# Kernel optimization log

Measured on AMD Instinct MI355X. Metric: run time of the kernel, lower is better.

## Reference

```python
import jax, jax.numpy as jnp
import numpy as np

B, H, LQ, LK, D = 2, 16, 2048, 2048, 128

def setup_inputs() -> dict:
    key = jax.random.key(0)
    k1, k2, k3 = jax.random.split(key, 3)
    q = jax.random.normal(k1, (B, H, LQ, D), dtype=jnp.float32)
    k = jax.random.normal(k2, (B, H, LK, D), dtype=jnp.float32)
    v = jax.random.normal(k3, (B, H, LK, D), dtype=jnp.float32)
    return {"q": q, "k": k, "v": v}

def reference(q, k, v):
    # scaled dot-product attention: softmax(q k^T / sqrt(D)) v
    scale = q.shape[-1] ** (-0.5)
    # scores: [B,H,Lq,Lk]
    scores = jnp.einsum('bhqd,bhkd->bhqk', q, k) * scale
    attn = jax.nn.softmax(scores, axis=-1)
    out = jnp.einsum('bhqk,bhkd->bhqd', attn, v)  # [B,H,Lq,Dv]
    return out
```

## Files before the change

kernel.cpp:

```cpp
#include <hip/hip_runtime.h>
#include <hip/hip_bf16.h>
#include <cstdint>

#define LQ_N   2048
#define LK_N   2048
#define DD     128
#define NHEADS 32
#define QBLK   128
#define KVBLK  64
#define NKV    (LK_N / KVBLK)
#define NQB    (LQ_N / QBLK)
#define SCALE  0.08838834764831845f
#define SCALE2 0.1275525003267101f

#define KTILE_BYTES (KVBLK * DD * 2)
#define WS_K_BYTES  ((size_t)NHEADS * NKV * KTILE_BYTES)
#define WS_NEED     (2 * WS_K_BYTES)

#define PSTR 72

typedef __attribute__((ext_vector_type(8)))  short bf16x8;
typedef __attribute__((ext_vector_type(4)))  float f32x4;
typedef __attribute__((ext_vector_type(16))) float f32x16;

#if __has_builtin(__builtin_amdgcn_exp2f)
#define EXP2F __builtin_amdgcn_exp2f
#else
#define EXP2F exp2f
#endif

__device__ inline unsigned short f2bf(float f) {
    union { float f; unsigned u; } x; x.f = f;
    unsigned r = (x.u + 0x7fffu + ((x.u >> 16) & 1u)) >> 16;
    return (unsigned short)r;
}

__device__ inline unsigned cvt_pk_bf16(float lo, float hi) {
    unsigned r;
    asm("v_cvt_pk_bf16_f32 %0, %1, %2" : "=v"(r) : "v"(lo), "v"(hi));
    return r;
}

__device__ inline bf16x8 make_pfrag(float v0, float v1, float v2, float v3,
                                    float v4, float v5, float v6, float v7) {
    unsigned a0 = cvt_pk_bf16(v0, v1);
    unsigned a1 = cvt_pk_bf16(v2, v3);
    unsigned b0 = cvt_pk_bf16(v4, v5);
    unsigned b1 = cvt_pk_bf16(v6, v7);
    asm volatile("v_permlane32_swap_b32 %0, %1" : "+v"(a0), "+v"(b0));
    asm volatile("v_permlane32_swap_b32 %0, %1" : "+v"(a1), "+v"(b1));
    union { unsigned u[4]; bf16x8 v8; } u;
    u.u[0] = a0; u.u[1] = a1; u.u[2] = b0; u.u[3] = b1;
    return u.v8;
}

__global__ __launch_bounds__(256, 2)
void prep_k_kernel(const float* __restrict__ K, char* __restrict__ ws)
{
    const int tid  = threadIdx.x;
    const int kvt  = blockIdx.x;
    const int head = blockIdx.y;
    const float* Kh = K + ((size_t)head * LK_N + (size_t)kvt * KVBLK) * DD;
    char* dst = ws + ((size_t)head * NKV + kvt) * KTILE_BYTES;
    #pragma unroll
    for (int i = 0; i < 4; ++i) {
        int c = tid + 256 * i;
        int row  = c >> 4;
        int col8 = c & 15;
        const float* src = Kh + (size_t)row * DD + col8 * 8;
        float4 a = *(const float4*)src;
        float4 b = *(const float4*)(src + 4);
        bf16x8 t;
        t[0] = (short)f2bf(a.x * SCALE2); t[1] = (short)f2bf(a.y * SCALE2);
        t[2] = (short)f2bf(a.z * SCALE2); t[3] = (short)f2bf(a.w * SCALE2);
        t[4] = (short)f2bf(b.x * SCALE2); t[5] = (short)f2bf(b.y * SCALE2);
        t[6] = (short)f2bf(b.z * SCALE2); t[7] = (short)f2bf(b.w * SCALE2);
        *(bf16x8*)(dst + row * 256 + ((col8 * 16) ^ ((row & 7) << 4))) = t;
    }
}

__global__ __launch_bounds__(256, 2)
void prep_vt_kernel(const float* __restrict__ V, char* __restrict__ ws)
{
    __shared__ unsigned short vt[DD * PSTR];
    const int tid  = threadIdx.x;
    const int kvt  = blockIdx.x;
    const int head = blockIdx.y;
    const float* Vh = V + ((size_t)head * LK_N + (size_t)kvt * KVBLK) * DD;
    #pragma unroll
    for (int i = 0; i < 8; ++i) {
        int f = tid + 256 * i;
        int r  = f >> 5;
        int c4 = f & 31;
        float4 x = *(const float4*)(Vh + (size_t)r * DD + c4 * 4);
        vt[(c4 * 4 + 0) * PSTR + r] = f2bf(x.x);
        vt[(c4 * 4 + 1) * PSTR + r] = f2bf(x.y);
        vt[(c4 * 4 + 2) * PSTR + r] = f2bf(x.z);
        vt[(c4 * 4 + 3) * PSTR + r] = f2bf(x.w);
    }
    __syncthreads();
    char* dst = ws + WS_K_BYTES + ((size_t)head * NKV + kvt) * KTILE_BYTES;
    #pragma unroll
    for (int i = 0; i < 4; ++i) {
        int c = tid + 256 * i;
        int d   = c >> 3;
        int kv8 = c & 7;
        bf16x8 t = *(const bf16x8*)&vt[d * PSTR + kv8 * 8];
        *(bf16x8*)(dst + d * 128 + ((kv8 * 16) ^ ((d & 7) << 4))) = t;
    }
}

__global__ __launch_bounds__(256, 2)
void attn_main_kernel(const float* __restrict__ Q, const char* __restrict__ kws,
                      const char* __restrict__ vws, float* __restrict__ O)
{
    __shared__ unsigned short kt_lds[KVBLK * DD];
    __shared__ unsigned short vt_lds[DD * KVBLK];

    const int tid  = threadIdx.x;
    const int lane = tid & 63;
    const int wave = tid >> 6;
    const int l31  = lane & 31;
    const int h    = lane >> 5;

    const int bid  = blockIdx.x;
    const int sid  = (bid & 7) * (NQB * NHEADS / 8) + (bid >> 3);
    const int head = sid >> 4;
    const int qb   = sid & 15;

    const float* Qh = Q + (size_t)head * LQ_N * DD;
    float*       Oh = O + (size_t)head * LQ_N * DD;
    const char*  kt_g = kws + (size_t)head * NKV * KTILE_BYTES;
    const char*  vt_g = vws + (size_t)head * NKV * KTILE_BYTES;

    const int qrow = qb * QBLK + wave * 32 + l31;
    bf16x8 qf[8];
    {
        const float* qp = Qh + (size_t)qrow * DD + 8 * h;
        #pragma unroll
        for (int kd = 0; kd < 8; ++kd) {
            float4 a = *(const float4*)(qp + 16 * kd);
            float4 b = *(const float4*)(qp + 16 * kd + 4);
            bf16x8 t;
            t[0] = (short)f2bf(a.x); t[1] = (short)f2bf(a.y);
            t[2] = (short)f2bf(a.z); t[3] = (short)f2bf(a.w);
            t[4] = (short)f2bf(b.x); t[5] = (short)f2bf(b.y);
            t[6] = (short)f2bf(b.z); t[7] = (short)f2bf(b.w);
            qf[kd] = t;
        }
    }

    f32x16 o_acc[4];
    #pragma unroll
    for (int nt = 0; nt < 4; ++nt)
        #pragma unroll
        for (int i = 0; i < 16; ++i) o_acc[nt][i] = 0.f;
    float m_run = -1e30f, l_run = 0.f;

    const bf16x8* kg = (const bf16x8*)kt_g;
    const bf16x8* vg = (const bf16x8*)vt_g;
    bf16x8 skreg[4], svreg[4];
    #pragma unroll
    for (int i = 0; i < 4; ++i) { skreg[i] = kg[tid + 256 * i]; svreg[i] = vg[tid + 256 * i]; }

    const char* kb = (const char*)kt_lds;
    const char* vb = (const char*)vt_lds;
    const int swz = (l31 & 7) << 4;

    for (int t = 0; t < NKV; ++t) {
        __syncthreads();
        #pragma unroll
        for (int i = 0; i < 4; ++i) {
            *(bf16x8*)&kt_lds[(tid + 256 * i) * 8] = skreg[i];
            *(bf16x8*)&vt_lds[(tid + 256 * i) * 8] = svreg[i];
        }
        __syncthreads();

        if (t + 1 < NKV) {
            int base = (t + 1) * (KTILE_BYTES / 16);
            #pragma unroll
            for (int i = 0; i < 4; ++i) {
                skreg[i] = kg[base + tid + 256 * i];
                svreg[i] = vg[base + tid + 256 * i];
            }
        }

        f32x16 s0, s1;
        #pragma unroll
        for (int i = 0; i < 16; ++i) { s0[i] = 0.f; s1[i] = 0.f; }
        __builtin_amdgcn_s_setprio(1);
        #pragma unroll
        for (int kd = 0; kd < 8; ++kd) {
            bf16x8 kf0 = *(const bf16x8*)(kb + l31 * 256        + ((32 * kd + 16 * h) ^ swz));
            bf16x8 kf1 = *(const bf16x8*)(kb + (32 + l31) * 256 + ((32 * kd + 16 * h) ^ swz));
            s0 = __builtin_amdgcn_mfma_f32_32x32x16_bf16(kf0, qf[kd], s0, 0, 0, 0);
            s1 = __builtin_amdgcn_mfma_f32_32x32x16_bf16(kf1, qf[kd], s1, 0, 0, 0);
        }
        __builtin_amdgcn_s_setprio(0);

        float pmax = s0[0];
        #pragma unroll
        for (int i = 1; i < 16; ++i) pmax = fmaxf(pmax, s0[i]);
        #pragma unroll
        for (int i = 0; i < 16; ++i) pmax = fmaxf(pmax, s1[i]);
        pmax = fmaxf(pmax, __shfl_xor(pmax, 32));

        if (!__all(pmax <= m_run + 8.0f)) {
            float mn = fmaxf(m_run, pmax);
            float al = EXP2F(m_run - mn);
            m_run = mn;
            l_run *= al;
            #pragma unroll
            for (int nt = 0; nt < 4; ++nt)
                #pragma unroll
                for (int i = 0; i < 16; ++i) o_acc[nt][i] *= al;
        }
        float sum = 0.f;
        #pragma unroll
        for (int i = 0; i < 16; ++i) { s0[i] = EXP2F(s0[i] - m_run); sum += s0[i]; }
        #pragma unroll
        for (int i = 0; i < 16; ++i) { s1[i] = EXP2F(s1[i] - m_run); sum += s1[i]; }
        sum += __shfl_xor(sum, 32);
        l_run += sum;

        bf16x8 pf0 = make_pfrag(s0[0], s0[1], s0[2],  s0[3],  s0[4],  s0[5],  s0[6],  s0[7]);
        bf16x8 pf1 = make_pfrag(s0[8], s0[9], s0[10], s0[11], s0[12], s0[13], s0[14], s0[15]);
        bf16x8 pf2 = make_pfrag(s1[0], s1[1], s1[2],  s1[3],  s1[4],  s1[5],  s1[6],  s1[7]);
        bf16x8 pf3 = make_pfrag(s1[8], s1[9], s1[10], s1[11], s1[12], s1[13], s1[14], s1[15]);

        __builtin_amdgcn_s_setprio(1);
        #pragma unroll
        for (int nt = 0; nt < 4; ++nt) {
            int d = 32 * nt + l31;
            const char* vrow = vb + d * 128;
            bf16x8 vf0 = *(const bf16x8*)(vrow + ((16 * h      ) ^ swz));
            bf16x8 vf1 = *(const bf16x8*)(vrow + ((32 + 16 * h ) ^ swz));
            bf16x8 vf2 = *(const bf16x8*)(vrow + ((64 + 16 * h ) ^ swz));
            bf16x8 vf3 = *(const bf16x8*)(vrow + ((96 + 16 * h ) ^ swz));
            o_acc[nt] = __builtin_amdgcn_mfma_f32_32x32x16_bf16(vf0, pf0, o_acc[nt], 0, 0, 0);
            o_acc[nt] = __builtin_amdgcn_mfma_f32_32x32x16_bf16(vf1, pf1, o_acc[nt], 0, 0, 0);
            o_acc[nt] = __builtin_amdgcn_mfma_f32_32x32x16_bf16(vf2, pf2, o_acc[nt], 0, 0, 0);
            o_acc[nt] = __builtin_amdgcn_mfma_f32_32x32x16_bf16(vf3, pf3, o_acc[nt], 0, 0, 0);
        }
        __builtin_amdgcn_s_setprio(0);
    }

    float inv = 1.0f / l_run;
    float* op = Oh + (size_t)qrow * DD;
    #pragma unroll
    for (int nt = 0; nt < 4; ++nt)
        #pragma unroll
        for (int p = 0; p < 4; ++p) {
            int dbase = 32 * nt + 8 * p + 4 * h;
            float4 w;
            w.x = o_acc[nt][4 * p + 0] * inv;
            w.y = o_acc[nt][4 * p + 1] * inv;
            w.z = o_acc[nt][4 * p + 2] * inv;
            w.w = o_acc[nt][4 * p + 3] * inv;
            *(float4*)(op + dbase) = w;
        }
}

#define KSTRIDE  136
#define VTSTRIDE 40
#define FKV 32

__global__ __launch_bounds__(256, 2)
void attn_fwd_fallback(const float* __restrict__ Q, const float* __restrict__ K,
                       const float* __restrict__ V, float* __restrict__ O)
{
    __shared__ unsigned short k_lds[FKV * KSTRIDE];
    __shared__ unsigned short vt_lds[DD * VTSTRIDE];
    __shared__ unsigned short p_lds2[4 * 16 * VTSTRIDE];

    const int tid  = threadIdx.x;
    const int lane = tid & 63;
    const int wave = tid >> 6;
    const int head = blockIdx.y;
    const int qb   = blockIdx.x;

    const float* Qh = Q + (size_t)head * LQ_N * DD;
    const float* Kh = K + (size_t)head * LK_N * DD;
    const float* Vh = V + (size_t)head * LK_N * DD;
    float*       Oh = O + (size_t)head * LQ_N * DD;

    const int r16 = lane & 15;
    const int g   = lane >> 4;

    const int qrow = qb * 64 + wave * 16 + r16;
    bf16x8 qf[4];
    {
        const float* qp = Qh + (size_t)qrow * DD + 8 * g;
        #pragma unroll
        for (int kt = 0; kt < 4; ++kt) {
            float4 a = *(const float4*)(qp + 32 * kt);
            float4 b = *(const float4*)(qp + 32 * kt + 4);
            bf16x8 t;
            t[0] = (short)f2bf(a.x * SCALE); t[1] = (short)f2bf(a.y * SCALE);
            t[2] = (short)f2bf(a.z * SCALE); t[3] = (short)f2bf(a.w * SCALE);
            t[4] = (short)f2bf(b.x * SCALE); t[5] = (short)f2bf(b.y * SCALE);
            t[6] = (short)f2bf(b.z * SCALE); t[7] = (short)f2bf(b.w * SCALE);
            qf[kt] = t;
        }
    }

    f32x4 o_acc[8];
    #pragma unroll
    for (int dt = 0; dt < 8; ++dt) o_acc[dt] = (f32x4){0.f, 0.f, 0.f, 0.f};
    float m_run[4], l_run[4];
    #pragma unroll
    for (int r = 0; r < 4; ++r) { m_run[r] = -1e30f; l_run[r] = 0.f; }

    for (int kv = 0; kv < LK_N / FKV; ++kv) {
        const float* Kt = Kh + (size_t)kv * FKV * DD;
        const float* Vt = Vh + (size_t)kv * FKV * DD;
        __syncthreads();
        #pragma unroll
        for (int i = 0; i < 4; ++i) {
            int f = tid + 256 * i;
            int row = f >> 5, colf = f & 31;
            float4 x = *(const float4*)(Kt + (size_t)row * DD + colf * 4);
            ushort4 pk;
            pk.x = f2bf(x.x); pk.y = f2bf(x.y); pk.z = f2bf(x.z); pk.w = f2bf(x.w);
            *(ushort4*)(&k_lds[row * KSTRIDE + colf * 4]) = pk;
        }
        #pragma unroll
        for (int i = 0; i < 4; ++i) {
            int f = tid + 256 * i;
            int row = f >> 5, colf = f & 31;
            float4 x = *(const float4*)(Vt + (size_t)row * DD + colf * 4);
            vt_lds[(colf * 4 + 0) * VTSTRIDE + row] = f2bf(x.x);
            vt_lds[(colf * 4 + 1) * VTSTRIDE + row] = f2bf(x.y);
            vt_lds[(colf * 4 + 2) * VTSTRIDE + row] = f2bf(x.z);
            vt_lds[(colf * 4 + 3) * VTSTRIDE + row] = f2bf(x.w);
        }
        __syncthreads();

        f32x4 s0 = (f32x4){0.f,0.f,0.f,0.f};
        f32x4 s1 = (f32x4){0.f,0.f,0.f,0.f};
        #pragma unroll
        for (int kt = 0; kt < 4; ++kt) {
            bf16x8 kf0 = *(const bf16x8*)&k_lds[(r16)      * KSTRIDE + 32 * kt + 8 * g];
            bf16x8 kf1 = *(const bf16x8*)&k_lds[(16 + r16) * KSTRIDE + 32 * kt + 8 * g];
            s0 = __builtin_amdgcn_mfma_f32_16x16x32_bf16(qf[kt], kf0, s0, 0, 0, 0);
            s1 = __builtin_amdgcn_mfma_f32_16x16x32_bf16(qf[kt], kf1, s1, 0, 0, 0);
        }

        float alpha[4];
        f32x4 p0, p1;
        #pragma unroll
        for (int r = 0; r < 4; ++r) {
            float t = fmaxf(s0[r], s1[r]);
            t = fmaxf(t, __shfl_xor(t, 1));
            t = fmaxf(t, __shfl_xor(t, 2));
            t = fmaxf(t, __shfl_xor(t, 4));
            t = fmaxf(t, __shfl_xor(t, 8));
            float mn = fmaxf(m_run[r], t);
            alpha[r] = __expf(m_run[r] - mn);
            m_run[r] = mn;
            p0[r] = __expf(s0[r] - mn);
            p1[r] = __expf(s1[r] - mn);
            float su = p0[r] + p1[r];
            su += __shfl_xor(su, 1);
            su += __shfl_xor(su, 2);
            su += __shfl_xor(su, 4);
            su += __shfl_xor(su, 8);
            l_run[r] = l_run[r] * alpha[r] + su;
        }

        unsigned short* pw = &p_lds2[wave * 16 * VTSTRIDE];
        #pragma unroll
        for (int r = 0; r < 4; ++r) {
            int row = 4 * g + r;
            pw[row * VTSTRIDE + r16]      = f2bf(p0[r]);
            pw[row * VTSTRIDE + 16 + r16] = f2bf(p1[r]);
        }
        bf16x8 pf = *(const bf16x8*)&pw[r16 * VTSTRIDE + 8 * g];

        #pragma unroll
        for (int dt = 0; dt < 8; ++dt) {
            #pragma unroll
            for (int r = 0; r < 4; ++r) o_acc[dt][r] *= alpha[r];
        }
        #pragma unroll
        for (int dt = 0; dt < 8; ++dt) {
            bf16x8 vf = *(const bf16x8*)&vt_lds[(16 * dt + r16) * VTSTRIDE + 8 * g];
            o_acc[dt] = __builtin_amdgcn_mfma_f32_16x16x32_bf16(pf, vf, o_acc[dt], 0, 0, 0);
        }
    }

    #pragma unroll
    for (int r = 0; r < 4; ++r) {
        float inv = 1.0f / l_run[r];
        int row = qb * 64 + wave * 16 + 4 * g + r;
        float* op = Oh + (size_t)row * DD + r16;
        #pragma unroll
        for (int dt = 0; dt < 8; ++dt)
            op[16 * dt] = o_acc[dt][r] * inv;
    }
}

extern "C" void kernel_launch(void* const* d_in, const int* in_sizes, int n_in,
                              void* d_out, int out_size, void* d_ws, size_t ws_size,
                              hipStream_t stream) {
    const float* q = (const float*)d_in[0];
    const float* k = (const float*)d_in[1];
    const float* v = (const float*)d_in[2];
    float* o = (float*)d_out;

    if (ws_size >= WS_NEED) {
        char* ws = (char*)d_ws;
        prep_k_kernel <<<dim3(NKV, NHEADS), 256, 0, stream>>>(k, ws);
        prep_vt_kernel<<<dim3(NKV, NHEADS), 256, 0, stream>>>(v, ws);
        attn_main_kernel<<<dim3(NQB * NHEADS), 256, 0, stream>>>(
            q, ws, ws + WS_K_BYTES, o);
    } else {
        attn_fwd_fallback<<<dim3(LQ_N / 64, NHEADS), 256, 0, stream>>>(q, k, v, o);
    }
}
```

Baseline: 104.1 us.

## Stream K/V tiles directly into double-buffered LDS with global_load_lds

The main loop now loads K and V tiles with direct global-to-LDS transfers into two LDS buffers, issued two tiles ahead. This replaces the register staging and LDS store path and the two barriers per iteration. The prep kernels now write tiles in a column-group-major, 16-byte-chunk order that matches lane-contiguous LDS reads, dropping the XOR swizzle. This removes register pressure and VGPR-to-LDS write traffic, at the cost of doubled LDS usage (64KB per block, 2 blocks/CU) and hand-written vmcnt waits that must stay correct.

```diff
diff --git a/kernel.cpp b/kernel.cpp
--- a/kernel.cpp
+++ b/kernel.cpp
@@ -54,20 +54,27 @@
     return u.v8;
 }
 
+__device__ inline void gld16(const char* g, const char* l) {
+    __builtin_amdgcn_global_load_lds(
+        (const __attribute__((address_space(1))) unsigned int*)g,
+        (__attribute__((address_space(3))) unsigned int*)l,
+        16, 0, 0);
+}
+
 __global__ __launch_bounds__(256, 2)
 void prep_k_kernel(const float* __restrict__ K, char* __restrict__ ws)
 {
+    __shared__ unsigned short kt[KVBLK * 136];
     const int tid  = threadIdx.x;
     const int kvt  = blockIdx.x;
     const int head = blockIdx.y;
     const float* Kh = K + ((size_t)head * LK_N + (size_t)kvt * KVBLK) * DD;
-    char* dst = ws + ((size_t)head * NKV + kvt) * KTILE_BYTES;
     #pragma unroll
     for (int i = 0; i < 4; ++i) {
         int c = tid + 256 * i;
-        int row  = c >> 4;
-        int col8 = c & 15;
-        const float* src = Kh + (size_t)row * DD + col8 * 8;
+        int r  = c >> 4;
+        int c8 = c & 15;
+        const float* src = Kh + (size_t)r * DD + c8 * 8;
         float4 a = *(const float4*)src;
         float4 b = *(const float4*)(src + 4);
         bf16x8 t;
@@ -75,7 +82,17 @@
         t[2] = (short)f2bf(a.z * SCALE2); t[3] = (short)f2bf(a.w * SCALE2);
         t[4] = (short)f2bf(b.x * SCALE2); t[5] = (short)f2bf(b.y * SCALE2);
         t[6] = (short)f2bf(b.z * SCALE2); t[7] = (short)f2bf(b.w * SCALE2);
-        *(bf16x8*)(dst + row * 256 + ((col8 * 16) ^ ((row & 7) << 4))) = t;
+        *(bf16x8*)&kt[r * 136 + c8 * 8] = t;
+    }
+    __syncthreads();
+    char* dst = ws + ((size_t)head * NKV + kvt) * KTILE_BYTES;
+    #pragma unroll
+    for (int i = 0; i < 4; ++i) {
+        int c = tid + 256 * i;
+        int g = c >> 6;
+        int r = c & 63;
+        bf16x8 t = *(const bf16x8*)&kt[r * 136 + g * 8];
+        *(bf16x8*)(dst + c * 16) = t;
     }
 }
 
@@ -103,10 +120,10 @@
     #pragma unroll
     for (int i = 0; i < 4; ++i) {
         int c = tid + 256 * i;
-        int d   = c >> 3;
-        int kv8 = c & 7;
-        bf16x8 t = *(const bf16x8*)&vt[d * PSTR + kv8 * 8];
-        *(bf16x8*)(dst + d * 128 + ((kv8 * 16) ^ ((d & 7) << 4))) = t;
+        int g = c >> 7;
+        int d = c & 127;
+        bf16x8 t = *(const bf16x8*)&vt[d * PSTR + g * 8];
+        *(bf16x8*)(dst + c * 16) = t;
     }
 }
 
@@ -114,8 +131,8 @@
 void attn_main_kernel(const float* __restrict__ Q, const char* __restrict__ kws,
                       const char* __restrict__ vws, float* __restrict__ O)
 {
-    __shared__ unsigned short kt_lds[KVBLK * DD];
-    __shared__ unsigned short vt_lds[DD * KVBLK];
+    __shared__ unsigned short kt_lds[2][KVBLK * DD];
+    __shared__ unsigned short vt_lds[2][DD * KVBLK];
 
     const int tid  = threadIdx.x;
     const int lane = tid & 63;
@@ -149,6 +166,7 @@
             qf[kd] = t;
         }
     }
+    asm volatile("s_waitcnt vmcnt(0)" ::: "memory");
 
     f32x16 o_acc[4];
     #pragma unroll
@@ -157,33 +175,28 @@
         for (int i = 0; i < 16; ++i) o_acc[nt][i] = 0.f;
     float m_run = -1e30f, l_run = 0.f;
 
-    const bf16x8* kg = (const bf16x8*)kt_g;
-    const bf16x8* vg = (const bf16x8*)vt_g;
-    bf16x8 skreg[4], svreg[4];
-    #pragma unroll
-    for (int i = 0; i < 4; ++i) { skreg[i] = kg[tid + 256 * i]; svreg[i] = vg[tid + 256 * i]; }
-
-    const char* kb = (const char*)kt_lds;
-    const char* vb = (const char*)vt_lds;
-    const int swz = (l31 & 7) << 4;
+    auto issue = [&](int t, int b) {
+        const char* ks = kt_g + (size_t)t * KTILE_BYTES;
+        const char* vs = vt_g + (size_t)t * KTILE_BYTES;
+        const char* kl = (const char*)&kt_lds[b][0];
+        const char* vl = (const char*)&vt_lds[b][0];
+        #pragma unroll
+        for (int i = 0; i < 4; ++i) {
+            int off = (tid + 256 * i) * 16;
+            gld16(ks + off, kl + off);
+            gld16(vs + off, vl + off);
+        }
+    };
+    issue(0, 0);
+    issue(1, 1);
 
     for (int t = 0; t < NKV; ++t) {
-        __syncthreads();
-        #pragma unroll
-        for (int i = 0; i < 4; ++i) {
-            *(bf16x8*)&kt_lds[(tid + 256 * i) * 8] = skreg[i];
-            *(bf16x8*)&vt_lds[(tid + 256 * i) * 8] = svreg[i];
-        }
-        __syncthreads();
-
-        if (t + 1 < NKV) {
-            int base = (t + 1) * (KTILE_BYTES / 16);
-            #pragma unroll
-            for (int i = 0; i < 4; ++i) {
-                skreg[i] = kg[base + tid + 256 * i];
-                svreg[i] = vg[base + tid + 256 * i];
-            }
-        }
+        if (t < NKV - 1) asm volatile("s_waitcnt vmcnt(8)" ::: "memory");
+        else             asm volatile("s_waitcnt vmcnt(0)" ::: "memory");
+        __builtin_amdgcn_s_barrier();
+
+        const char* kb = (const char*)&kt_lds[t & 1][0];
+        const char* vb = (const char*)&vt_lds[t & 1][0];
 
         f32x16 s0, s1;
         #pragma unroll
@@ -191,8 +204,9 @@
         __builtin_amdgcn_s_setprio(1);
         #pragma unroll
         for (int kd = 0; kd < 8; ++kd) {
-            bf16x8 kf0 = *(const bf16x8*)(kb + l31 * 256        + ((32 * kd + 16 * h) ^ swz));
-            bf16x8 kf1 = *(const bf16x8*)(kb + (32 + l31) * 256 + ((32 * kd + 16 * h) ^ swz));
+            int g = 2 * kd + h;
+            bf16x8 kf0 = *(const bf16x8*)(kb + ((g * 64 + l31) << 4));
+            bf16x8 kf1 = *(const bf16x8*)(kb + ((g * 64 + 32 + l31) << 4));
             s0 = __builtin_amdgcn_mfma_f32_32x32x16_bf16(kf0, qf[kd], s0, 0, 0, 0);
             s1 = __builtin_amdgcn_mfma_f32_32x32x16_bf16(kf1, qf[kd], s1, 0, 0, 0);
         }
@@ -232,17 +246,19 @@
         #pragma unroll
         for (int nt = 0; nt < 4; ++nt) {
             int d = 32 * nt + l31;
-            const char* vrow = vb + d * 128;
-            bf16x8 vf0 = *(const bf16x8*)(vrow + ((16 * h      ) ^ swz));
-            bf16x8 vf1 = *(const bf16x8*)(vrow + ((32 + 16 * h ) ^ swz));
-            bf16x8 vf2 = *(const bf16x8*)(vrow + ((64 + 16 * h ) ^ swz));
-            bf16x8 vf3 = *(const bf16x8*)(vrow + ((96 + 16 * h ) ^ swz));
+            bf16x8 vf0 = *(const bf16x8*)(vb + (((0 + h) * 128 + d) << 4));
+            bf16x8 vf1 = *(const bf16x8*)(vb + (((2 + h) * 128 + d) << 4));
+            bf16x8 vf2 = *(const bf16x8*)(vb + (((4 + h) * 128 + d) << 4));
+            bf16x8 vf3 = *(const bf16x8*)(vb + (((6 + h) * 128 + d) << 4));
             o_acc[nt] = __builtin_amdgcn_mfma_f32_32x32x16_bf16(vf0, pf0, o_acc[nt], 0, 0, 0);
             o_acc[nt] = __builtin_amdgcn_mfma_f32_32x32x16_bf16(vf1, pf1, o_acc[nt], 0, 0, 0);
             o_acc[nt] = __builtin_amdgcn_mfma_f32_32x32x16_bf16(vf2, pf2, o_acc[nt], 0, 0, 0);
             o_acc[nt] = __builtin_amdgcn_mfma_f32_32x32x16_bf16(vf3, pf3, o_acc[nt], 0, 0, 0);
         }
         __builtin_amdgcn_s_setprio(0);
+
+        __builtin_amdgcn_s_barrier();
+        if (t + 2 < NKV) issue(t + 2, t & 1);
     }
 
     float inv = 1.0f / l_run;
```

New measurement: 101.1 us. -2.9%, faster.
